# Optimization experiments

Hardware: AMD Instinct MI355X
Metric: run time of the kernel (lower is better)

The kernel has to match this reference:

```python
import jax, jax.numpy as jnp
import numpy as np

V, D = 100000, 128
B, W, K = 16384, 10, 10


def setup_inputs() -> dict:
    key = jax.random.key(0)
    k1, k2, k3, k4, k5 = jax.random.split(key, 5)
    init_range = 0.5 / D
    return {
        "context": jax.random.randint(k1, (B, W), 0, V, dtype=jnp.int64 if jax.config.jax_enable_x64 else jnp.int32),
        "target": jax.random.randint(k2, (B,), 0, V, dtype=jnp.int64 if jax.config.jax_enable_x64 else jnp.int32),
        "noise": jax.random.randint(k3, (B, K), 0, V, dtype=jnp.int64 if jax.config.jax_enable_x64 else jnp.int32),
        "emb_w": jax.random.uniform(k4, (V, D), jnp.float32, -init_range, init_range),
        "ctx_w": jax.random.uniform(k5, (V, D), jnp.float32, -init_range, init_range),
    }


def reference(context, target, noise, emb_w, ctx_w):
    # Gather + mean-pool context embeddings: [B, W, D] -> [B, D]
    context_vec = ctx_w[context].mean(axis=1)
    # Target embeddings: [B, D]
    target_vec = emb_w[target]
    # Original does matmul(target_vec, context_vec.T).diag(); same math as row-wise dot.
    pos_score = jax.nn.log_sigmoid(jnp.einsum("bd,bd->b", target_vec, context_vec))  # [B]
    # Negative samples: [B, K, D] x [B, D] -> [B, K], then log-sigmoid and sum -> [B, 1]
    noise_vec = emb_w[noise]
    neg_score = jax.nn.log_sigmoid(jnp.einsum("bkd,bd->bk", noise_vec, context_vec)).sum(axis=1, keepdims=True)  # [B, 1]
    # Faithful to torch broadcasting bug: [B] + [B,1] -> [B,B], then mean.
    return -(pos_score[None, :] + neg_score).mean()
```

## Files before the change

### kernel.cpp

```cpp
#include <hip/hip_runtime.h>
#include <hip/hip_bf16.h>
#include <math.h>


#define CBOW_B 16384
#define CBOW_W 10
#define CBOW_K 10
#define CBOW_D 128
#define ROWS_PER_BLOCK 8
#define NBLOCKS (CBOW_B / ROWS_PER_BLOCK)

__device__ __forceinline__ float log_sigmoid(float x) {
    const float t = __expf(-fabsf(x));
    return fminf(x, 0.0f) - __logf(1.0f + t);
}

__global__ __launch_bounds__(256) void cbow_main(
    const int* __restrict__ context,
    const int* __restrict__ target,
    const int* __restrict__ noise,
    const float* __restrict__ emb_w,
    const float* __restrict__ ctx_w,
    float* __restrict__ block_sums)
{
    const int wave = threadIdx.x >> 6;
    const int lane = threadIdx.x & 63;
    const int grp  = lane >> 5;
    const int sub  = lane & 31;
    const int b = blockIdx.x * ROWS_PER_BLOCK + wave * 2 + grp;
    const unsigned elem = sub * 4u;

    const int2* cI = reinterpret_cast<const int2*>(&context[b * CBOW_W]);
    const int2 c01 = cI[0], c23 = cI[1], c45 = cI[2], c67 = cI[3], c89 = cI[4];
    const int2* nI = reinterpret_cast<const int2*>(&noise[b * CBOW_K]);
    const int2 n01 = nI[0], n23 = nI[1], n45 = nI[2], n67 = nI[3], n89 = nI[4];
    const int tgt = target[b];

    float cx = 0, cy = 0, cz = 0, cw = 0;
    #define CBOW_ACC(IDX) {                                                    \
        const float4 r = *reinterpret_cast<const float4*>(                     \
            ctx_w + ((unsigned)(IDX) * (unsigned)CBOW_D + elem));              \
        cx += r.x; cy += r.y; cz += r.z; cw += r.w; }
    CBOW_ACC(c01.x) CBOW_ACC(c01.y) CBOW_ACC(c23.x) CBOW_ACC(c23.y)
    CBOW_ACC(c45.x) CBOW_ACC(c45.y) CBOW_ACC(c67.x) CBOW_ACC(c67.y)
    CBOW_ACC(c89.x) CBOW_ACC(c89.y)
    #undef CBOW_ACC
    const float inv = 1.0f / CBOW_W;
    cx *= inv; cy *= inv; cz *= inv; cw *= inv;

    float sum = 0.0f;
    #define CBOW_DOT(IDX) {                                                    \
        const float4 r = *reinterpret_cast<const float4*>(                     \
            emb_w + ((unsigned)(IDX) * (unsigned)CBOW_D + elem));              \
        float p = cx * r.x + cy * r.y + cz * r.z + cw * r.w;                   \
        p += __shfl_xor(p, 1, 64);                                             \
        p += __shfl_xor(p, 2, 64);                                             \
        p += __shfl_xor(p, 4, 64);                                             \
        p += __shfl_xor(p, 8, 64);                                             \
        p += __shfl_xor(p, 16, 64);                                            \
        sum += log_sigmoid(p); }
    CBOW_DOT(tgt)
    CBOW_DOT(n01.x) CBOW_DOT(n01.y) CBOW_DOT(n23.x) CBOW_DOT(n23.y)
    CBOW_DOT(n45.x) CBOW_DOT(n45.y) CBOW_DOT(n67.x) CBOW_DOT(n67.y)
    CBOW_DOT(n89.x) CBOW_DOT(n89.y)
    #undef CBOW_DOT

    sum += __shfl_xor(sum, 32, 64);

    __shared__ float wsum[4];
    if (lane == 0) wsum[wave] = sum;
    __syncthreads();
    if (threadIdx.x == 0) {
        float s = 0.0f;
        #pragma unroll
        for (int i = 0; i < 4; ++i) s += wsum[i];
        block_sums[blockIdx.x] = s;
    }
}

__global__ __launch_bounds__(256) void cbow_finish(
    const float* __restrict__ block_sums, float* __restrict__ out)
{
    __shared__ double sh[256];
    double s = 0.0;
    for (int i = threadIdx.x; i < NBLOCKS; i += 256) s += (double)block_sums[i];
    sh[threadIdx.x] = s;
    __syncthreads();
    #pragma unroll
    for (int stride = 128; stride >= 1; stride >>= 1) {
        if (threadIdx.x < stride) sh[threadIdx.x] += sh[threadIdx.x + stride];
        __syncthreads();
    }
    if (threadIdx.x == 0) {
        out[0] = (float)(-sh[0] / (double)CBOW_B);
    }
}

extern "C" void kernel_launch(void* const* d_in, const int* in_sizes, int n_in,
                              void* d_out, int out_size, void* d_ws, size_t ws_size,
                              hipStream_t stream) {
    const int*   context = (const int*)d_in[0];
    const int*   target  = (const int*)d_in[1];
    const int*   noise   = (const int*)d_in[2];
    const float* emb_w   = (const float*)d_in[3];
    const float* ctx_w   = (const float*)d_in[4];
    float*       out     = (float*)d_out;
    float*       block_sums = (float*)d_ws;

    cbow_main<<<NBLOCKS, 256, 0, stream>>>(context, target, noise, emb_w, ctx_w,
                                           block_sums);
    cbow_finish<<<1, 256, 0, stream>>>(block_sums, out);
}
```

Baseline: 34.93 us.

## Fuse final reduction via last-block atomic and use 16 lanes per row

Merges the separate finish kernel into the main kernel: each block writes its partial sum, bumps an atomic counter, and the last block to finish performs the final double-precision reduction. Each row is now handled by 16 lanes loading two float4s each instead of 32 lanes with one float4, so each block covers 16 rows and there are half as many blocks. This aims to remove a kernel launch and cut shuffle steps, but adds a memset launch plus an atomic and threadfence per block.

```diff
diff --git a/kernel.cpp b/kernel.cpp
--- a/kernel.cpp
+++ b/kernel.cpp
@@ -7,7 +7,7 @@
 #define CBOW_W 10
 #define CBOW_K 10
 #define CBOW_D 128
-#define ROWS_PER_BLOCK 8
+#define ROWS_PER_BLOCK 16
 #define NBLOCKS (CBOW_B / ROWS_PER_BLOCK)
 
 __device__ __forceinline__ float log_sigmoid(float x) {
@@ -15,20 +15,22 @@
     return fminf(x, 0.0f) - __logf(1.0f + t);
 }
 
-__global__ __launch_bounds__(256) void cbow_main(
+__global__ __launch_bounds__(256) void cbow_fused(
     const int* __restrict__ context,
     const int* __restrict__ target,
     const int* __restrict__ noise,
     const float* __restrict__ emb_w,
     const float* __restrict__ ctx_w,
-    float* __restrict__ block_sums)
+    float* __restrict__ block_sums,
+    int* __restrict__ done_count,
+    float* __restrict__ out)
 {
     const int wave = threadIdx.x >> 6;
     const int lane = threadIdx.x & 63;
-    const int grp  = lane >> 5;
-    const int sub  = lane & 31;
-    const int b = blockIdx.x * ROWS_PER_BLOCK + wave * 2 + grp;
-    const unsigned elem = sub * 4u;
+    const int grp  = lane >> 4;
+    const int sub  = lane & 15;
+    const int b = blockIdx.x * ROWS_PER_BLOCK + wave * 4 + grp;
+    const unsigned elem = sub * 8u;
 
     const int2* cI = reinterpret_cast<const int2*>(&context[b * CBOW_W]);
     const int2 c01 = cI[0], c23 = cI[1], c45 = cI[2], c67 = cI[3], c89 = cI[4];
@@ -36,54 +38,62 @@
     const int2 n01 = nI[0], n23 = nI[1], n45 = nI[2], n67 = nI[3], n89 = nI[4];
     const int tgt = target[b];
 
-    float cx = 0, cy = 0, cz = 0, cw = 0;
+    float c0x=0,c0y=0,c0z=0,c0w=0, c1x=0,c1y=0,c1z=0,c1w=0;
     #define CBOW_ACC(IDX) {                                                    \
-        const float4 r = *reinterpret_cast<const float4*>(                     \
-            ctx_w + ((unsigned)(IDX) * (unsigned)CBOW_D + elem));              \
-        cx += r.x; cy += r.y; cz += r.z; cw += r.w; }
+        const float4* p = reinterpret_cast<const float4*>(                     \
+            ctx_w + (((unsigned)(IDX) << 7) + elem));                          \
+        const float4 r0 = p[0];                                                \
+        const float4 r1 = p[1];                                                \
+        c0x += r0.x; c0y += r0.y; c0z += r0.z; c0w += r0.w;                    \
+        c1x += r1.x; c1y += r1.y; c1z += r1.z; c1w += r1.w; }
     CBOW_ACC(c01.x) CBOW_ACC(c01.y) CBOW_ACC(c23.x) CBOW_ACC(c23.y)
     CBOW_ACC(c45.x) CBOW_ACC(c45.y) CBOW_ACC(c67.x) CBOW_ACC(c67.y)
     CBOW_ACC(c89.x) CBOW_ACC(c89.y)
     #undef CBOW_ACC
     const float inv = 1.0f / CBOW_W;
-    cx *= inv; cy *= inv; cz *= inv; cw *= inv;
+    c0x*=inv; c0y*=inv; c0z*=inv; c0w*=inv;
+    c1x*=inv; c1y*=inv; c1z*=inv; c1w*=inv;
 
     float sum = 0.0f;
     #define CBOW_DOT(IDX) {                                                    \
-        const float4 r = *reinterpret_cast<const float4*>(                     \
-            emb_w + ((unsigned)(IDX) * (unsigned)CBOW_D + elem));              \
-        float p = cx * r.x + cy * r.y + cz * r.z + cw * r.w;                   \
-        p += __shfl_xor(p, 1, 64);                                             \
-        p += __shfl_xor(p, 2, 64);                                             \
-        p += __shfl_xor(p, 4, 64);                                             \
-        p += __shfl_xor(p, 8, 64);                                             \
-        p += __shfl_xor(p, 16, 64);                                            \
-        sum += log_sigmoid(p); }
+        const float4* p = reinterpret_cast<const float4*>(                     \
+            emb_w + (((unsigned)(IDX) << 7) + elem));                          \
+        const float4 r0 = p[0];                                                \
+        const float4 r1 = p[1];                                                \
+        float d = c0x*r0.x + c0y*r0.y + c0z*r0.z + c0w*r0.w                    \
+                + c1x*r1.x + c1y*r1.y + c1z*r1.z + c1w*r1.w;                   \
+        d += __shfl_xor(d, 1, 64);                                             \
+        d += __shfl_xor(d, 2, 64);                                             \
+        d += __shfl_xor(d, 4, 64);                                             \
+        d += __shfl_xor(d, 8, 64);                                             \
+        sum += log_sigmoid(d); }
     CBOW_DOT(tgt)
     CBOW_DOT(n01.x) CBOW_DOT(n01.y) CBOW_DOT(n23.x) CBOW_DOT(n23.y)
     CBOW_DOT(n45.x) CBOW_DOT(n45.y) CBOW_DOT(n67.x) CBOW_DOT(n67.y)
     CBOW_DOT(n89.x) CBOW_DOT(n89.y)
     #undef CBOW_DOT
 
+    sum += __shfl_xor(sum, 16, 64);
     sum += __shfl_xor(sum, 32, 64);
 
     __shared__ float wsum[4];
+    __shared__ int is_last;
     if (lane == 0) wsum[wave] = sum;
     __syncthreads();
     if (threadIdx.x == 0) {
-        float s = 0.0f;
-        #pragma unroll
-        for (int i = 0; i < 4; ++i) s += wsum[i];
-        block_sums[blockIdx.x] = s;
+        block_sums[blockIdx.x] = wsum[0] + wsum[1] + wsum[2] + wsum[3];
+        __threadfence();
+        const int old = atomicAdd(done_count, 1);
+        is_last = (old == NBLOCKS - 1);
     }
-}
+    __syncthreads();
+    if (!is_last) return;
 
-__global__ __launch_bounds__(256) void cbow_finish(
-    const float* __restrict__ block_sums, float* __restrict__ out)
-{
+    __threadfence();
     __shared__ double sh[256];
     double s = 0.0;
-    for (int i = threadIdx.x; i < NBLOCKS; i += 256) s += (double)block_sums[i];
+    for (int i = threadIdx.x; i < NBLOCKS; i += 256)
+        s += (double)block_sums[i];
     sh[threadIdx.x] = s;
     __syncthreads();
     #pragma unroll
@@ -106,8 +116,9 @@
     const float* ctx_w   = (const float*)d_in[4];
     float*       out     = (float*)d_out;
     float*       block_sums = (float*)d_ws;
+    int*         done_count = (int*)d_ws + NBLOCKS;
 
-    cbow_main<<<NBLOCKS, 256, 0, stream>>>(context, target, noise, emb_w, ctx_w,
-                                           block_sums);
-    cbow_finish<<<1, 256, 0, stream>>>(block_sums, out);
+    hipMemsetAsync(done_count, 0, sizeof(int), stream);
+    cbow_fused<<<NBLOCKS, 256, 0, stream>>>(context, target, noise, emb_w, ctx_w,
+                                            block_sums, done_count, out);
 }
```

Result: slower. 67.82 us (+94.1%).
